# Kernel tuning notes

Measured on AMD Instinct MI355X. Metric: run time of the kernel, lower is better.

The kernel has to match this reference:

```python
import jax, jax.numpy as jnp
import numpy as np

PC = 512      # proposal_channels == conv_channels
INCH = 512    # in_channels of branch
B = 8
T = 64        # pyramid level length (feat_t) at order=0
TF = 256      # frame_level_feature length (clip_length)
KERNELS = [8, 16, 8, 4, 2, 2, 2]  # ConPoolingKernal
CLC = 498     # feature_lastclass channels (CLC + 2 == 500)
GROUPS = 32


def _gn(x, gamma, beta):
    # GroupNorm(32, C) over [B, C, L]
    Bb, C, L = x.shape
    xg = x.reshape(Bb, GROUPS, C // GROUPS, L)
    m = xg.mean(axis=(2, 3), keepdims=True)
    v = xg.var(axis=(2, 3), keepdims=True)
    xn = ((xg - m) * jax.lax.rsqrt(v + 1e-5)).reshape(Bb, C, L)
    return xn * gamma[None, :, None] + beta[None, :, None]


def _c1(x, w, b):
    # Unit1D kernel_shape=1: pointwise conv
    return jnp.einsum('bct,oc->bot', x, w) + b[None, :, None]


def _bmp(feat, segs):
    # BoundaryMaxPooling: first C/2 channels max-pooled over segs[...,0:2],
    # second C/2 over segs[...,2:4] (inclusive integer ranges, clamped).
    Bb, C, L = feat.shape
    C2 = C // 2
    pos = jnp.arange(L)
    def pool(f, s, e):
        s = jnp.clip(s, 0, L - 1)
        e = jnp.maximum(jnp.clip(e, 0, L - 1), s)
        mask = (pos[None, None, :] >= s[..., None]) & (pos[None, None, :] <= e[..., None])  # [B,T,L]
        return jnp.max(jnp.where(mask[:, None], f[:, :, None, :], -jnp.inf), axis=-1)  # [B,C2,T]
    return jnp.concatenate([pool(feat[:, :C2], segs[..., 0], segs[..., 1]),
                            pool(feat[:, C2:], segs[..., 2], segs[..., 3])], axis=1)


def _anchor_gather(feat, anc, K):
    # Vectorized per-anchor clamp/slice + nearest F.interpolate(size=K):
    # src index for output k of a slice [l, r] is l + floor(k * (r - l + 1) / K).
    Bb, C, L = feat.shape
    left = jnp.clip(anc[..., 0], 0, L)
    right = jnp.clip(anc[..., 1], 0, L)
    valid = right > left                      # empty slices -> zeros (torch branch)
    seglen = right + 1 - left
    k = jnp.arange(K)
    idx = jnp.clip(left[..., None] + (k[None, None, :] * seglen[..., None]) // K, 0, L - 1)  # [B,T,K]
    g = jax.vmap(lambda f, ix: f[:, ix])(feat, idx)   # [B,C,T,K]
    return g * valid[:, None, :, None].astype(feat.dtype)


def setup_inputs() -> dict:
    key = jax.random.key(0)
    ks = jax.random.split(key, 16)
    f32 = jnp.float32
    s = 0.02
    def w(k, shape):
        return jax.random.normal(k, shape, f32) * s
    inp = {}
    inp['feature'] = jax.random.normal(ks[0], (B, INCH, T), f32)
    inp['frame_level_feature'] = jax.random.normal(ks[1], (B, PC, TF), f32)
    inp['segments'] = jax.random.randint(ks[2], (B, T, 4), 0, T).astype(jnp.int32)
    inp['frame_segments'] = jax.random.randint(ks[3], (B, T, 4), 0, TF).astype(jnp.int32)
    inp['feature_lastclass'] = jax.random.normal(ks[4], (B, CLC, T), f32)
    inp['anchor'] = jnp.sort(jax.random.randint(ks[5], (B, T, 2), 0, T), axis=-1).astype(jnp.int32)
    inp['frame_anchor'] = jnp.sort(jax.random.randint(ks[6], (B, T, 2), 0, TF), axis=-1).astype(jnp.int32)
    inp['order'] = 0
    inp['LocResult_feature'] = jax.random.normal(ks[7], (B, 2, T), f32)
    inp['w_cur'] = w(ks[8], (PC, INCH)); inp['b_cur'] = jnp.zeros((PC,), f32)
    inp['g_cur'] = jnp.ones((PC,), f32); inp['be_cur'] = jnp.zeros((PC,), f32)
    inp['w_lr'] = w(ks[9], (2 * PC, INCH)); inp['b_lr'] = jnp.zeros((2 * PC,), f32)
    inp['g_lr'] = jnp.ones((2 * PC,), f32); inp['be_lr'] = jnp.zeros((2 * PC,), f32)
    inp['w_roi'] = w(ks[10], (PC, PC)); inp['b_roi'] = jnp.zeros((PC,), f32)
    inp['g_roi'] = jnp.ones((PC,), f32); inp['be_roi'] = jnp.zeros((PC,), f32)
    K1 = KERNELS[1]; K0 = KERNELS[0]
    inp['w_cp'] = w(ks[11], (PC, 2 * PC, K1)); inp['b_cp'] = jnp.zeros((PC,), f32)
    inp['w_cp0'] = w(ks[12], (PC, PC, K0)); inp['b_cp0'] = jnp.zeros((PC,), f32)
    CIN = 6 * PC + 500
    inp['w_prop'] = w(ks[13], (INCH, CIN)); inp['b_prop'] = jnp.zeros((INCH,), f32)
    inp['g_prop'] = jnp.ones((INCH,), f32); inp['be_prop'] = jnp.zeros((INCH,), f32)
    return inp


def reference(feature, frame_level_feature, segments, frame_segments, feature_lastclass,
              anchor, frame_anchor, order, LocResult_feature,
              w_cur, b_cur, g_cur, be_cur, w_lr, b_lr, g_lr, be_lr,
              w_roi, b_roi, g_roi, be_roi, w_cp, b_cp, w_cp0, b_cp0,
              w_prop, b_prop, g_prop, be_prop):
    relu = jax.nn.relu
    fm_short = relu(_gn(_c1(feature, w_cur, b_cur), g_cur, be_cur))           # [B,PC,T]
    feat_lr = relu(_gn(_c1(feature, w_lr, b_lr), g_lr, be_lr))                # [B,2PC,T]
    prop_feature = _bmp(feat_lr, segments)                                    # [B,2PC,T]
    prop_roi = relu(_gn(_c1(_bmp(frame_level_feature, frame_segments), w_roi, b_roi), g_roi, be_roi))
    K1 = KERNELS[order + 1]
    K0 = KERNELS[0]
    g1 = _anchor_gather(feat_lr, anchor, K1)                                  # [B,2PC,T,K1]
    con_feature = jnp.einsum('bctk,ock->bot', g1, w_cp) + b_cp[None, :, None]  # valid conv K1->1
    g0 = _anchor_gather(frame_level_feature, frame_anchor, K0)                # [B,PC,T,K0]
    frame_con = jnp.einsum('bctk,ock->bot', g0, w_cp0) + b_cp0[None, :, None]
    prop_con = relu(_gn(_c1(frame_con, w_roi, b_roi), g_roi, be_roi))
    cat = jnp.concatenate([prop_roi, prop_feature, fm_short, feature_lastclass,
                           con_feature, prop_con, LocResult_feature], axis=1)  # [B,6PC+500,T]
    out = relu(_gn(_c1(cat, w_prop, b_prop), g_prop, be_prop))                # [B,INCH,T]
    return (out, feat_lr)
```

## Files before the change

kernel.cpp:

```cpp
#include <hip/hip_runtime.h>
#include <math.h>

#define BB 8
#define CATP 3584
#define CAT_REAL 3572

typedef __attribute__((ext_vector_type(8))) short short8;
typedef __attribute__((ext_vector_type(4))) float f32x4;

__device__ inline ushort f2bf(float f) {
  union { float f; unsigned u; } x;
  x.f = f;
  return (ushort)((x.u + 0x7FFFu + ((x.u >> 16) & 1u)) >> 16);
}
__device__ inline float bf2f(unsigned us) {
  union { unsigned u; float f; } x;
  x.u = us << 16;
  return x.f;
}

template <int Cin, int Kf>
__device__ void cpT_tile(const float* __restrict__ W, ushort* __restrict__ D,
                         int nt, int cc) {
  const int tid = threadIdx.x;
  const int j = tid >> 6, l4 = (tid >> 4) & 3, l15 = tid & 15;
  const int o = nt * 64 + j * 16 + l15;
  const int cb = cc * 32 + l4 * 8;
  ushort rg[8][Kf];
#pragma unroll
  for (int q = 0; q < 8; q++) {
    const float* row = W + ((size_t)o * Cin + cb + q) * Kf;
#pragma unroll
    for (int kq = 0; kq < Kf / 4; kq++) {
      const float4 f = *(const float4*)(row + kq * 4);
      rg[q][kq * 4 + 0] = f2bf(f.x);
      rg[q][kq * 4 + 1] = f2bf(f.y);
      rg[q][kq * 4 + 2] = f2bf(f.z);
      rg[q][kq * 4 + 3] = f2bf(f.w);
    }
  }
#pragma unroll
  for (int k = 0; k < Kf; k++) {
    uint4 pk;
    pk.x = (unsigned)rg[0][k] | ((unsigned)rg[1][k] << 16);
    pk.y = (unsigned)rg[2][k] | ((unsigned)rg[3][k] << 16);
    pk.z = (unsigned)rg[4][k] | ((unsigned)rg[5][k] << 16);
    pk.w = (unsigned)rg[6][k] | ((unsigned)rg[7][k] << 16);
    *(uint4*)(D + ((size_t)(nt * Kf + k) * (Cin >> 5) + cc) * 2048 + tid * 8) = pk;
  }
}

__global__ __launch_bounds__(256) void prep_kernel(
    const float* __restrict__ w_cur, const float* __restrict__ w_lr,
    const float* __restrict__ w_roi, const float* __restrict__ w_prop,
    ushort* __restrict__ Wcomb, ushort* __restrict__ Wroi,
    ushort* __restrict__ Wprop, const float* __restrict__ w_cp,
    ushort* __restrict__ WcpT, const float* __restrict__ w_cp0,
    ushort* __restrict__ Wcp0T, const float* __restrict__ feature,
    const float* __restrict__ frame_feat, const float* __restrict__ lastcls,
    const float* __restrict__ locres, ushort* __restrict__ Ft,
    ushort* __restrict__ FfT, ushort* __restrict__ cat) {
  __shared__ float tile[64 * 65];
  const int bid = blockIdx.x;
  if (bid < 1408) {
    const int i = bid * 256 + threadIdx.x;
    const float* src;
    ushort* dst;
    int o, k8, Kc;
    bool pad = false;
    if (i < 98304) {
      o = i >> 6; k8 = i & 63; Kc = 16;
      src = (o < 512) ? (w_cur + (size_t)o * 512)
                      : (w_lr + (size_t)(o - 512) * 512);
      dst = Wcomb;
    } else if (i < 131072) {
      const int r = i - 98304;
      o = r >> 6; k8 = r & 63; Kc = 16;
      src = w_roi + (size_t)o * 512;
      dst = Wroi;
    } else {
      const int r = i - 131072;
      if (r >= 229376) return;
      o = r / 448; k8 = r % 448; Kc = 112;
      src = w_prop + (size_t)o * CAT_REAL;
      dst = Wprop;
      pad = true;
    }
    const int k = k8 * 8;
    float v[8];
    if (pad) {
#pragma unroll
      for (int q = 0; q < 8; q++) v[q] = (k + q < CAT_REAL) ? src[k + q] : 0.f;
    } else {
      const float4 f0 = *(const float4*)(src + k);
      const float4 f1 = *(const float4*)(src + k + 4);
      v[0] = f0.x; v[1] = f0.y; v[2] = f0.z; v[3] = f0.w;
      v[4] = f1.x; v[5] = f1.y; v[6] = f1.z; v[7] = f1.w;
    }
    uint4 pk;
    pk.x = (unsigned)f2bf(v[0]) | ((unsigned)f2bf(v[1]) << 16);
    pk.y = (unsigned)f2bf(v[2]) | ((unsigned)f2bf(v[3]) << 16);
    pk.z = (unsigned)f2bf(v[4]) | ((unsigned)f2bf(v[5]) << 16);
    pk.w = (unsigned)f2bf(v[6]) | ((unsigned)f2bf(v[7]) << 16);
    const int ot = o >> 6, ii = (o >> 4) & 3, l15 = o & 15;
    const int kc = k8 >> 2, l4 = k8 & 3;
    const size_t flat =
        ((((size_t)ot * Kc + kc) * 4 + ii) * 64 + l4 * 16 + l15) * 8;
    *(uint4*)(dst + flat) = pk;
    return;
  }
  if (bid < 1792) {
    const int local = bid - 1408;
    if (local < 256)
      cpT_tile<1024, 16>(w_cp, WcpT, local >> 5, local & 31);
    else {
      const int r = local - 256;
      cpT_tile<512, 8>(w_cp0, Wcp0T, r >> 4, r & 15);
    }
    return;
  }
  const int local = bid - 1792;
  const float* src;
  ushort* dst;
  int Cr, Cw, L, rs, co, cblk, lblk, b;
  if (local < 64) {
    src = feature; dst = Ft; Cr = 512; Cw = 512; L = 64; rs = 512; co = 0;
    cblk = local & 7; lblk = 0; b = local >> 3;
  } else if (local < 320) {
    const int r = local - 64;
    src = frame_feat; dst = FfT; Cr = 512; Cw = 512; L = 256; rs = 512; co = 0;
    cblk = r & 7; lblk = (r >> 3) & 3; b = r >> 5;
  } else if (local < 384) {
    const int r = local - 320;
    src = lastcls; dst = cat; Cr = 498; Cw = 498; L = 64; rs = CATP; co = 2048;
    cblk = r & 7; lblk = 0; b = r >> 3;
  } else {
    const int r = local - 384;
    src = locres; dst = cat; Cr = 2; Cw = 14; L = 64; rs = CATP; co = 3570;
    cblk = 0; lblk = 0; b = r;
  }
  const int c0 = cblk * 64, l0 = lblk * 64;
  for (int e = threadIdx.x; e < 4096; e += 256) {
    const int cc = e >> 6, ll = e & 63;
    const int c = c0 + cc;
    tile[cc * 65 + ll] = (c < Cr) ? src[((size_t)b * Cr + c) * L + l0 + ll] : 0.f;
  }
  __syncthreads();
  for (int e = threadIdx.x; e < 4096; e += 256) {
    const int ll = e >> 6, cc = e & 63;
    const int c = c0 + cc;
    if (c < Cw)
      dst[((size_t)b * L + l0 + ll) * rs + co + c] = f2bf(tile[cc * 65 + ll]);
  }
}

__global__ __launch_bounds__(256) void gemm_gn_seg_kernel(
    int nblk0,
    const ushort* __restrict__ X0, const ushort* __restrict__ W0,
    const float* __restrict__ b0, const float* __restrict__ g0,
    const float* __restrict__ e0, int Kp0, int cs0, float* of0, int om0,
    ushort* co0, int cst0, int coff0,
    const ushort* __restrict__ X1, const ushort* __restrict__ W1,
    const float* __restrict__ b1, const float* __restrict__ g1,
    const float* __restrict__ e1, int Kp1, int cs1, float* of1, int om1,
    ushort* co1, int cst1, int coff1) {
  const int bx = blockIdx.x;
  const bool s1 = bx >= nblk0;
  const ushort* Xt = s1 ? X1 : X0;
  const ushort* Wb = s1 ? W1 : W0;
  const float* bias = s1 ? b1 : b0;
  const float* gamma = s1 ? g1 : g0;
  const float* beta = s1 ? e1 : e0;
  const int Kp = s1 ? Kp1 : Kp0;
  const int cpgShift = s1 ? cs1 : cs0;
  float* outF = s1 ? of1 : of0;
  const int outFM = s1 ? om1 : om0;
  ushort* catOut = s1 ? co1 : co0;
  const int catStride = s1 ? cst1 : cst0;
  const int chOff = s1 ? coff1 : coff0;
  const int o0 = (s1 ? bx - nblk0 : bx) * 64;

  const int b = blockIdx.y;
  const int w = threadIdx.x >> 6;
  const int lane = threadIdx.x & 63;
  const int l15 = lane & 15, l4 = lane >> 4;
  const int wk = Kp >> 2;
  const int kbeg = w * wk, kend = kbeg + wk;

  f32x4 acc[4][4] = {};
  const ushort* wbase = Wb + (size_t)(o0 >> 6) * (Kp >> 5) * 2048 + lane * 8;
  const ushort* bp[4];
#pragma unroll
  for (int j = 0; j < 4; j++)
    bp[j] = Xt + (size_t)(b * 64 + j * 16 + l15) * Kp + l4 * 8;

  for (int k = kbeg; k < kend; k += 32) {
    const int kc = k >> 5;
    short8 a[4], x[4];
#pragma unroll
    for (int i = 0; i < 4; i++)
      a[i] = *(const short8*)(wbase + ((size_t)kc * 4 + i) * 512);
#pragma unroll
    for (int j = 0; j < 4; j++) x[j] = *(const short8*)(bp[j] + k);
#pragma unroll
    for (int i = 0; i < 4; i++)
#pragma unroll
      for (int j = 0; j < 4; j++)
        acc[i][j] = __builtin_amdgcn_mfma_f32_16x16x32_bf16(a[i], x[j],
                                                            acc[i][j], 0, 0, 0);
  }

  __shared__ float red[64 * 65];
  for (int ww = 0; ww < 4; ww++) {
    __syncthreads();
    if (w == ww) {
#pragma unroll
      for (int i = 0; i < 4; i++)
#pragma unroll
        for (int j = 0; j < 4; j++)
#pragma unroll
          for (int r = 0; r < 4; r++) {
            const int m = i * 16 + l4 * 4 + r;
            const int n = j * 16 + l15;
            if (ww == 0)
              red[m * 65 + n] = acc[i][j][r] + bias[o0 + m];
            else
              red[m * 65 + n] += acc[i][j][r];
          }
    }
  }
  __syncthreads();

  const int cpg = 1 << cpgShift;
  const int ngroups = 64 >> cpgShift;
  __shared__ float rs[4], rss[4], gmean[4], grstd[4];
  for (int gi = 0; gi < ngroups; gi++) {
    float s = 0.f, ss = 0.f;
    const int nel = cpg << 6;
    for (int e = threadIdx.x; e < nel; e += 256) {
      const float v = red[((gi << cpgShift) + (e >> 6)) * 65 + (e & 63)];
      s += v;
      ss += v * v;
    }
#pragma unroll
    for (int off = 32; off > 0; off >>= 1) {
      s += __shfl_down(s, off);
      ss += __shfl_down(ss, off);
    }
    if (lane == 0) { rs[w] = s; rss[w] = ss; }
    __syncthreads();
    if (threadIdx.x == 0) {
      const float ts = rs[0] + rs[1] + rs[2] + rs[3];
      const float tss = rss[0] + rss[1] + rss[2] + rss[3];
      const float mean = ts / (float)nel;
      const float var = tss / (float)nel - mean * mean;
      gmean[gi] = mean;
      grstd[gi] = rsqrtf(var + 1e-5f);
    }
    __syncthreads();
  }

  if (outF) {
    for (int e = threadIdx.x; e < 4096; e += 256) {
      const int m = e >> 6, n = e & 63;
      const int gi = m >> cpgShift;
      const int c = o0 + m;
      float v = (red[m * 65 + n] - gmean[gi]) * grstd[gi] * gamma[c] + beta[c];
      v = fmaxf(v, 0.f);
      outF[((size_t)b * outFM + c) * 64 + n] = v;
    }
  }
  if (catOut) {
    for (int e = threadIdx.x; e < 4096; e += 256) {
      const int n = e >> 6, m = e & 63;
      const int gi = m >> cpgShift;
      const int c = o0 + m;
      float v = (red[m * 65 + n] - gmean[gi]) * grstd[gi] * gamma[c] + beta[c];
      v = fmaxf(v, 0.f);
      catOut[((size_t)(b * 64) + n) * catStride + chOff + c] = f2bf(v);
    }
  }
}

__global__ __launch_bounds__(256) void gemm_part_kernel(
    const ushort* __restrict__ Xt, const ushort* __restrict__ Wb,
    float* __restrict__ P) {
  const int ot = blockIdx.x;
  const int b = blockIdx.y;
  const int kz = blockIdx.z;
  const int w = threadIdx.x >> 6;
  const int lane = threadIdx.x & 63;
  const int l15 = lane & 15, l4 = lane >> 4;
  const int kbeg = kz * 896 + w * 224;
  const int kend = kbeg + 224;

  f32x4 acc[4][4] = {};
  const ushort* wbase = Wb + (size_t)ot * (CATP >> 5) * 2048 + lane * 8;
  const ushort* bp[4];
#pragma unroll
  for (int j = 0; j < 4; j++)
    bp[j] = Xt + (size_t)(b * 64 + j * 16 + l15) * CATP + l4 * 8;

  for (int k = kbeg; k < kend; k += 32) {
    const int kc = k >> 5;
    short8 a[4], x[4];
#pragma unroll
    for (int i = 0; i < 4; i++)
      a[i] = *(const short8*)(wbase + ((size_t)kc * 4 + i) * 512);
#pragma unroll
    for (int j = 0; j < 4; j++) x[j] = *(const short8*)(bp[j] + k);
#pragma unroll
    for (int i = 0; i < 4; i++)
#pragma unroll
      for (int j = 0; j < 4; j++)
        acc[i][j] = __builtin_amdgcn_mfma_f32_16x16x32_bf16(a[i], x[j],
                                                            acc[i][j], 0, 0, 0);
  }

  __shared__ float red[64 * 65];
  for (int ww = 0; ww < 4; ww++) {
    __syncthreads();
    if (w == ww) {
#pragma unroll
      for (int i = 0; i < 4; i++)
#pragma unroll
        for (int j = 0; j < 4; j++)
#pragma unroll
          for (int r = 0; r < 4; r++) {
            const int m = i * 16 + l4 * 4 + r;
            const int n = j * 16 + l15;
            if (ww == 0)
              red[m * 65 + n] = acc[i][j][r];
            else
              red[m * 65 + n] += acc[i][j][r];
          }
    }
  }
  __syncthreads();
  float* Pp = P + (((size_t)kz * BB + b) * 512 + ot * 64) * 64;
  for (int e = threadIdx.x; e < 4096; e += 256) Pp[e] = red[(e >> 6) * 65 + (e & 63)];
}

__global__ __launch_bounds__(256) void reduce_gn_kernel(
    const float* __restrict__ P, const float* __restrict__ bias,
    const float* __restrict__ gamma, const float* __restrict__ beta,
    float* __restrict__ outF) {
  const int ot = blockIdx.x;
  const int b = blockIdx.y;
  const int o0 = ot * 64;
  const int w = threadIdx.x >> 6;
  const int lane = threadIdx.x & 63;
  __shared__ float red[64 * 65];
  for (int e = threadIdx.x; e < 4096; e += 256) {
    const int m = e >> 6, n = e & 63;
    float s = bias[o0 + m];
#pragma unroll
    for (int z = 0; z < 4; z++)
      s += P[(((size_t)z * BB + b) * 512 + o0 + m) * 64 + n];
    red[m * 65 + n] = s;
  }
  __syncthreads();
  __shared__ float rs[4], rss[4], gmean[4], grstd[4];
  for (int gi = 0; gi < 4; gi++) {
    float s = 0.f, ss = 0.f;
    for (int e = threadIdx.x; e < 1024; e += 256) {
      const float v = red[((gi << 4) + (e >> 6)) * 65 + (e & 63)];
      s += v;
      ss += v * v;
    }
#pragma unroll
    for (int off = 32; off > 0; off >>= 1) {
      s += __shfl_down(s, off);
      ss += __shfl_down(ss, off);
    }
    if (lane == 0) { rs[w] = s; rss[w] = ss; }
    __syncthreads();
    if (threadIdx.x == 0) {
      const float ts = rs[0] + rs[1] + rs[2] + rs[3];
      const float tss = rss[0] + rss[1] + rss[2] + rss[3];
      const float mean = ts / 1024.f;
      const float var = tss / 1024.f - mean * mean;
      gmean[gi] = mean;
      grstd[gi] = rsqrtf(var + 1e-5f);
    }
    __syncthreads();
  }
  for (int e = threadIdx.x; e < 4096; e += 256) {
    const int m = e >> 6, n = e & 63;
    const int gi = m >> 4;
    const int c = o0 + m;
    float v = (red[m * 65 + n] - gmean[gi]) * grstd[gi] * gamma[c] + beta[c];
    outF[((size_t)b * 512 + c) * 64 + n] = fmaxf(v, 0.f);
  }
}

template <int C, int L>
__device__ void bmp_body(const ushort* __restrict__ Xt,
                         const int* __restrict__ segs, ushort* __restrict__ Y,
                         int rowStride, int chOff, float2 (*pmax)[512]) {
  constexpr int C2 = C / 2;
  constexpr int P2 = C2 / 2;
  constexpr int CH = P2 / 64;
  const int t = blockIdx.x;
  const int b = blockIdx.y;
  const int w = threadIdx.x >> 6;
  const int lane = threadIdx.x & 63;
  const int* sg = segs + ((size_t)b * 64 + t) * 4;
  const ushort* Xb = Xt + (size_t)b * L * C;
#pragma unroll
  for (int h = 0; h < 2; h++) {
    const int s = min(max(sg[2 * h], 0), L - 1);
    const int e = max(min(max(sg[2 * h + 1], 0), L - 1), s);
#pragma unroll
    for (int q = 0; q < CH; q++) {
      const int p = q * 64 + lane;
      const ushort* base = Xb + h * C2 + 2 * p;
      float a0 = -INFINITY, a1 = -INFINITY;
      float c0 = -INFINITY, c1 = -INFINITY;
      int l = s + w;
      for (; l + 4 <= e; l += 8) {
        const unsigned u0 = *(const unsigned*)(base + (size_t)l * C);
        const unsigned u1 = *(const unsigned*)(base + (size_t)(l + 4) * C);
        a0 = fmaxf(a0, bf2f(u0 & 0xffffu));
        a1 = fmaxf(a1, bf2f(u0 >> 16));
        c0 = fmaxf(c0, bf2f(u1 & 0xffffu));
        c1 = fmaxf(c1, bf2f(u1 >> 16));
      }
      if (l <= e) {
        const unsigned u0 = *(const unsigned*)(base + (size_t)l * C);
        a0 = fmaxf(a0, bf2f(u0 & 0xffffu));
        a1 = fmaxf(a1, bf2f(u0 >> 16));
      }
      pmax[w][h * P2 + p] = make_float2(fmaxf(a0, c0), fmaxf(a1, c1));
    }
  }
  __syncthreads();
  for (int idx = threadIdx.x; idx < 2 * P2; idx += 256) {
    float2 m = pmax[0][idx];
#pragma unroll
    for (int ww = 1; ww < 4; ww++) {
      const float2 v = pmax[ww][idx];
      m.x = fmaxf(m.x, v.x);
      m.y = fmaxf(m.y, v.y);
    }
    const unsigned o = (unsigned)f2bf(m.x) | ((unsigned)f2bf(m.y) << 16);
    *(unsigned*)(Y + ((size_t)(b * 64) + t) * rowStride + chOff + 2 * idx) = o;
  }
}

__global__ __launch_bounds__(256) void bmp_dual_kernel(
    const ushort* __restrict__ FlrT, const int* __restrict__ segments,
    ushort* __restrict__ cat, const ushort* __restrict__ FfT,
    const int* __restrict__ frame_segs, ushort* __restrict__ XbmpT) {
  __shared__ float2 pm[4][512];
  if (blockIdx.z == 0)
    bmp_body<1024, 64>(FlrT, segments, cat, CATP, 512, pm);
  else
    bmp_body<512, 256>(FfT, frame_segs, XbmpT, 512, 0, pm);
}

template <int Kf, int L, int Cin>
__device__ void anchor_mfma_body(const ushort* __restrict__ src,
                                 const int* __restrict__ anc,
                                 const ushort* __restrict__ Wt,
                                 float* __restrict__ P, int slice, float* red) {
  const int nt = blockIdx.x;
  const int b = blockIdx.y;
  const int w = threadIdx.x >> 6;
  const int lane = threadIdx.x & 63;
  const int l15 = lane & 15, l4 = lane >> 4;
  const int kz = slice >> 1, chalf = slice & 1;
  const int k = kz * 4 + w;
  const int cbase = chalf * (Cin / 2);

  const ushort* rp[4];
#pragma unroll
  for (int i = 0; i < 4; i++) {
    const int t = i * 16 + l15;
    const int a0 = anc[((size_t)b * 64 + t) * 2 + 0];
    const int a1 = anc[((size_t)b * 64 + t) * 2 + 1];
    const int left = min(max(a0, 0), L);
    const int right = min(max(a1, 0), L);
    const int seglen = right + 1 - left;
    const int ix = min(max(left + (k * seglen) / Kf, 0), L - 1);
    rp[i] = src + ((size_t)b * L + ix) * Cin + cbase + l4 * 8;
  }
  const ushort* wb = Wt + (size_t)(nt * Kf + k) * (Cin >> 5) * 2048 + lane * 8;

  f32x4 acc[4][4] = {};
  for (int c0 = 0; c0 < Cin / 2; c0 += 32) {
    const int cc = (cbase + c0) >> 5;
    short8 a[4], bb[4];
#pragma unroll
    for (int i = 0; i < 4; i++) a[i] = *(const short8*)(rp[i] + c0);
#pragma unroll
    for (int j = 0; j < 4; j++)
      bb[j] = *(const short8*)(wb + ((size_t)cc * 4 + j) * 512);
#pragma unroll
    for (int i = 0; i < 4; i++)
#pragma unroll
      for (int j = 0; j < 4; j++)
        acc[i][j] = __builtin_amdgcn_mfma_f32_16x16x32_bf16(a[i], bb[j],
                                                            acc[i][j], 0, 0, 0);
  }

  for (int ww = 0; ww < 4; ww++) {
    __syncthreads();
    if (w == ww) {
#pragma unroll
      for (int i = 0; i < 4; i++)
#pragma unroll
        for (int j = 0; j < 4; j++)
#pragma unroll
          for (int r = 0; r < 4; r++) {
            const int m = i * 16 + l4 * 4 + r;
            const int n = j * 16 + l15;
            if (ww == 0)
              red[m * 65 + n] = acc[i][j][r];
            else
              red[m * 65 + n] += acc[i][j][r];
          }
    }
  }
  __syncthreads();
  float* Pp = P + (((size_t)slice * BB + b) * 512 + nt * 64) * 64;
  for (int e = threadIdx.x; e < 4096; e += 256) {
    const int n = e >> 6, m = e & 63;
    Pp[e] = red[m * 65 + n];
  }
}

__global__ __launch_bounds__(256) void anchor_mfma_dual_kernel(
    const ushort* __restrict__ FlrT, const int* __restrict__ anchor,
    const ushort* __restrict__ WcpT, float* __restrict__ P1,
    const ushort* __restrict__ FfT, const int* __restrict__ frame_anchor,
    const ushort* __restrict__ Wcp0T, float* __restrict__ P0) {
  __shared__ float red[64 * 65];
  const int z = blockIdx.z;
  if (z < 8)
    anchor_mfma_body<16, 64, 1024>(FlrT, anchor, WcpT, P1, z, red);
  else
    anchor_mfma_body<8, 256, 512>(FfT, frame_anchor, Wcp0T, P0, z - 8, red);
}

__device__ void anchor_reduce_body(const float* __restrict__ P, int ks,
                                   const float* __restrict__ bias,
                                   const int* __restrict__ anc, int L,
                                   ushort* __restrict__ Y, int rowStride,
                                   int chOff, float* tile, float* sval) {
  const int o0 = blockIdx.x * 64;
  const int b = blockIdx.y;
  if (threadIdx.x < 64) {
    const int t = threadIdx.x;
    const int a0 = anc[((size_t)b * 64 + t) * 2 + 0];
    const int a1 = anc[((size_t)b * 64 + t) * 2 + 1];
    const int left = min(max(a0, 0), L);
    const int right = min(max(a1, 0), L);
    sval[t] = (right > left) ? 1.f : 0.f;
  }
  __syncthreads();
  for (int e = threadIdx.x; e < 4096; e += 256) {
    const int nl = e >> 6, m = e & 63;
    const int n = o0 + nl;
    float s = 0.f;
    for (int z = 0; z < ks; z++)
      s += P[(((size_t)z * BB + b) * 512 + n) * 64 + m];
    tile[nl * 65 + m] = s * sval[m] + bias[n];
  }
  __syncthreads();
  for (int e = threadIdx.x; e < 4096; e += 256) {
    const int m = e >> 6, nl = e & 63;
    Y[((size_t)(b * 64) + m) * rowStride + chOff + o0 + nl] =
        f2bf(tile[nl * 65 + m]);
  }
}

__global__ __launch_bounds__(256) void anchor_reduce_dual_kernel(
    const float* __restrict__ P1, const float* __restrict__ b_cp,
    const int* __restrict__ anchor, ushort* __restrict__ cat,
    const float* __restrict__ P0, const float* __restrict__ b_cp0,
    const int* __restrict__ frame_anchor, ushort* __restrict__ FconT) {
  __shared__ float tile[64 * 65];
  __shared__ float sval[64];
  if (blockIdx.z == 0)
    anchor_reduce_body(P1, 8, b_cp, anchor, 64, cat, CATP, 2546, tile, sval);
  else
    anchor_reduce_body(P0, 4, b_cp0, frame_anchor, 256, FconT, 512, 0, tile, sval);
}

extern "C" void kernel_launch(void* const* d_in, const int* in_sizes, int n_in,
                              void* d_out, int out_size, void* d_ws,
                              size_t ws_size, hipStream_t stream) {
  const float* feature      = (const float*)d_in[0];
  const float* frame_feat   = (const float*)d_in[1];
  const int*   segments     = (const int*)d_in[2];
  const int*   frame_segs   = (const int*)d_in[3];
  const float* feat_lastcls = (const float*)d_in[4];
  const int*   anchor       = (const int*)d_in[5];
  const int*   frame_anchor = (const int*)d_in[6];
  const float* locres       = (const float*)d_in[8];
  const float* w_cur  = (const float*)d_in[9];
  const float* b_cur  = (const float*)d_in[10];
  const float* g_cur  = (const float*)d_in[11];
  const float* be_cur = (const float*)d_in[12];
  const float* w_lr   = (const float*)d_in[13];
  const float* b_lr   = (const float*)d_in[14];
  const float* g_lr   = (const float*)d_in[15];
  const float* be_lr  = (const float*)d_in[16];
  const float* w_roi  = (const float*)d_in[17];
  const float* b_roi  = (const float*)d_in[18];
  const float* g_roi  = (const float*)d_in[19];
  const float* be_roi = (const float*)d_in[20];
  const float* w_cp   = (const float*)d_in[21];
  const float* b_cp   = (const float*)d_in[22];
  const float* w_cp0  = (const float*)d_in[23];
  const float* b_cp0  = (const float*)d_in[24];
  const float* w_prop = (const float*)d_in[25];
  const float* b_prop = (const float*)d_in[26];
  const float* g_prop = (const float*)d_in[27];
  const float* be_prop= (const float*)d_in[28];

  float* out_main = (float*)d_out;
  float* feat_lr  = (float*)d_out + BB * 512 * 64;

  ushort* cat_t  = (ushort*)d_ws;
  ushort* Ft     = cat_t + 1835008;
  ushort* XbmpT  = Ft + 262144;
  ushort* FconT  = XbmpT + 262144;
  ushort* Wcomb  = FconT + 262144;
  ushort* Wroi   = Wcomb + 786432;
  ushort* Wprop  = Wroi + 262144;
  ushort* WcpT   = Wprop + 1835008;
  ushort* Wcp0T  = WcpT + 8388608;
  ushort* FlrT   = Wcp0T + 2097152;
  ushort* FfT    = FlrT + 524288;
  float*  P1     = (float*)(FfT + 1048576);
  float*  P0     = P1 + 2097152;
  float*  P9     = P0 + 1048576;

  prep_kernel<<<2184, 256, 0, stream>>>(
      w_cur, w_lr, w_roi, w_prop, Wcomb, Wroi, Wprop, w_cp, WcpT, w_cp0,
      Wcp0T, feature, frame_feat, feat_lastcls, locres, Ft, FfT, cat_t);

  gemm_gn_seg_kernel<<<dim3(24, BB), 256, 0, stream>>>(
      8,
      Ft, Wcomb, b_cur, g_cur, be_cur, 512, 4, nullptr, 0, cat_t, CATP, 1536,
      Ft, Wcomb + 512 * 512, b_lr, g_lr, be_lr, 512, 5, feat_lr, 1024, FlrT,
      1024, 0);

  bmp_dual_kernel<<<dim3(64, BB, 2), 256, 0, stream>>>(
      FlrT, segments, cat_t, FfT, frame_segs, XbmpT);

  anchor_mfma_dual_kernel<<<dim3(8, BB, 12), 256, 0, stream>>>(
      FlrT, anchor, WcpT, P1, FfT, frame_anchor, Wcp0T, P0);

  anchor_reduce_dual_kernel<<<dim3(8, BB, 2), 256, 0, stream>>>(
      P1, b_cp, anchor, cat_t, P0, b_cp0, frame_anchor, FconT);

  gemm_gn_seg_kernel<<<dim3(16, BB), 256, 0, stream>>>(
      8,
      XbmpT, Wroi, b_roi, g_roi, be_roi, 512, 4, nullptr, 0, cat_t, CATP, 0,
      FconT, Wroi, b_roi, g_roi, be_roi, 512, 4, nullptr, 0, cat_t, CATP, 3058);

  gemm_part_kernel<<<dim3(8, BB, 4), 256, 0, stream>>>(cat_t, Wprop, P9);

  reduce_gn_kernel<<<dim3(8, BB), 256, 0, stream>>>(
      P9, b_prop, g_prop, be_prop, out_main);
}
```

Before: 266.7 us.

## Regroup pipeline stages into dependency-level fused kernels to cut launches

Replaces the separate gemm_gn, bmp, anchor_mfma, anchor_reduce and second gemm_gn launches with three level kernels. Each level kernel dispatches independent stages by blockIdx.z. Stages now run together as soon as their inputs exist: the frame-anchor MFMA runs beside the first pointwise GEMM, and the frame-anchor reduce runs beside the BMP and feature-anchor MFMA. This removes two kernel launches and their serialization gaps and lets small stages fill idle CUs. In exchange, shared memory becomes one union sized for the largest stage, and some grid blocks exit immediately without doing work.

```diff
diff --git a/kernel.cpp b/kernel.cpp
--- a/kernel.cpp
+++ b/kernel.cpp
@@ -4,6 +4,7 @@
 #define BB 8
 #define CATP 3584
 #define CAT_REAL 3572
+#define SH_FLOATS 4240
 
 typedef __attribute__((ext_vector_type(8))) short short8;
 typedef __attribute__((ext_vector_type(4))) float f32x4;
@@ -154,33 +155,17 @@
   }
 }
 
-__global__ __launch_bounds__(256) void gemm_gn_seg_kernel(
-    int nblk0,
-    const ushort* __restrict__ X0, const ushort* __restrict__ W0,
-    const float* __restrict__ b0, const float* __restrict__ g0,
-    const float* __restrict__ e0, int Kp0, int cs0, float* of0, int om0,
-    ushort* co0, int cst0, int coff0,
-    const ushort* __restrict__ X1, const ushort* __restrict__ W1,
-    const float* __restrict__ b1, const float* __restrict__ g1,
-    const float* __restrict__ e1, int Kp1, int cs1, float* of1, int om1,
-    ushort* co1, int cst1, int coff1) {
-  const int bx = blockIdx.x;
-  const bool s1 = bx >= nblk0;
-  const ushort* Xt = s1 ? X1 : X0;
-  const ushort* Wb = s1 ? W1 : W0;
-  const float* bias = s1 ? b1 : b0;
-  const float* gamma = s1 ? g1 : g0;
-  const float* beta = s1 ? e1 : e0;
-  const int Kp = s1 ? Kp1 : Kp0;
-  const int cpgShift = s1 ? cs1 : cs0;
-  float* outF = s1 ? of1 : of0;
-  const int outFM = s1 ? om1 : om0;
-  ushort* catOut = s1 ? co1 : co0;
-  const int catStride = s1 ? cst1 : cst0;
-  const int chOff = s1 ? coff1 : coff0;
-  const int o0 = (s1 ? bx - nblk0 : bx) * 64;
-
-  const int b = blockIdx.y;
+__device__ void gemm_gn_body(
+    const ushort* __restrict__ Xt, const ushort* __restrict__ Wb,
+    const float* __restrict__ bias, const float* __restrict__ gamma,
+    const float* __restrict__ beta, int Kp, int cpgShift, float* outF,
+    int outFM, ushort* catOut, int catStride, int chOff, int o0, int b,
+    float* sh) {
+  float* red = sh;
+  float* rs = sh + 4160;
+  float* rss = sh + 4164;
+  float* gmean = sh + 4168;
+  float* grstd = sh + 4172;
   const int w = threadIdx.x >> 6;
   const int lane = threadIdx.x & 63;
   const int l15 = lane & 15, l4 = lane >> 4;
@@ -210,7 +195,6 @@
                                                             acc[i][j], 0, 0, 0);
   }
 
-  __shared__ float red[64 * 65];
   for (int ww = 0; ww < 4; ww++) {
     __syncthreads();
     if (w == ww) {
@@ -233,7 +217,6 @@
 
   const int cpg = 1 << cpgShift;
   const int ngroups = 64 >> cpgShift;
-  __shared__ float rs[4], rss[4], gmean[4], grstd[4];
   for (int gi = 0; gi < ngroups; gi++) {
     float s = 0.f, ss = 0.f;
     const int nel = cpg << 6;
@@ -282,122 +265,10 @@
   }
 }
 
-__global__ __launch_bounds__(256) void gemm_part_kernel(
-    const ushort* __restrict__ Xt, const ushort* __restrict__ Wb,
-    float* __restrict__ P) {
-  const int ot = blockIdx.x;
-  const int b = blockIdx.y;
-  const int kz = blockIdx.z;
-  const int w = threadIdx.x >> 6;
-  const int lane = threadIdx.x & 63;
-  const int l15 = lane & 15, l4 = lane >> 4;
-  const int kbeg = kz * 896 + w * 224;
-  const int kend = kbeg + 224;
-
-  f32x4 acc[4][4] = {};
-  const ushort* wbase = Wb + (size_t)ot * (CATP >> 5) * 2048 + lane * 8;
-  const ushort* bp[4];
-#pragma unroll
-  for (int j = 0; j < 4; j++)
-    bp[j] = Xt + (size_t)(b * 64 + j * 16 + l15) * CATP + l4 * 8;
-
-  for (int k = kbeg; k < kend; k += 32) {
-    const int kc = k >> 5;
-    short8 a[4], x[4];
-#pragma unroll
-    for (int i = 0; i < 4; i++)
-      a[i] = *(const short8*)(wbase + ((size_t)kc * 4 + i) * 512);
-#pragma unroll
-    for (int j = 0; j < 4; j++) x[j] = *(const short8*)(bp[j] + k);
-#pragma unroll
-    for (int i = 0; i < 4; i++)
-#pragma unroll
-      for (int j = 0; j < 4; j++)
-        acc[i][j] = __builtin_amdgcn_mfma_f32_16x16x32_bf16(a[i], x[j],
-                                                            acc[i][j], 0, 0, 0);
-  }
-
-  __shared__ float red[64 * 65];
-  for (int ww = 0; ww < 4; ww++) {
-    __syncthreads();
-    if (w == ww) {
-#pragma unroll
-      for (int i = 0; i < 4; i++)
-#pragma unroll
-        for (int j = 0; j < 4; j++)
-#pragma unroll
-          for (int r = 0; r < 4; r++) {
-            const int m = i * 16 + l4 * 4 + r;
-            const int n = j * 16 + l15;
-            if (ww == 0)
-              red[m * 65 + n] = acc[i][j][r];
-            else
-              red[m * 65 + n] += acc[i][j][r];
-          }
-    }
-  }
-  __syncthreads();
-  float* Pp = P + (((size_t)kz * BB + b) * 512 + ot * 64) * 64;
-  for (int e = threadIdx.x; e < 4096; e += 256) Pp[e] = red[(e >> 6) * 65 + (e & 63)];
-}
-
-__global__ __launch_bounds__(256) void reduce_gn_kernel(
-    const float* __restrict__ P, const float* __restrict__ bias,
-    const float* __restrict__ gamma, const float* __restrict__ beta,
-    float* __restrict__ outF) {
-  const int ot = blockIdx.x;
-  const int b = blockIdx.y;
-  const int o0 = ot * 64;
-  const int w = threadIdx.x >> 6;
-  const int lane = threadIdx.x & 63;
-  __shared__ float red[64 * 65];
-  for (int e = threadIdx.x; e < 4096; e += 256) {
-    const int m = e >> 6, n = e & 63;
-    float s = bias[o0 + m];
-#pragma unroll
-    for (int z = 0; z < 4; z++)
-      s += P[(((size_t)z * BB + b) * 512 + o0 + m) * 64 + n];
-    red[m * 65 + n] = s;
-  }
-  __syncthreads();
-  __shared__ float rs[4], rss[4], gmean[4], grstd[4];
-  for (int gi = 0; gi < 4; gi++) {
-    float s = 0.f, ss = 0.f;
-    for (int e = threadIdx.x; e < 1024; e += 256) {
-      const float v = red[((gi << 4) + (e >> 6)) * 65 + (e & 63)];
-      s += v;
-      ss += v * v;
-    }
-#pragma unroll
-    for (int off = 32; off > 0; off >>= 1) {
-      s += __shfl_down(s, off);
-      ss += __shfl_down(ss, off);
-    }
-    if (lane == 0) { rs[w] = s; rss[w] = ss; }
-    __syncthreads();
-    if (threadIdx.x == 0) {
-      const float ts = rs[0] + rs[1] + rs[2] + rs[3];
-      const float tss = rss[0] + rss[1] + rss[2] + rss[3];
-      const float mean = ts / 1024.f;
-      const float var = tss / 1024.f - mean * mean;
-      gmean[gi] = mean;
-      grstd[gi] = rsqrtf(var + 1e-5f);
-    }
-    __syncthreads();
-  }
-  for (int e = threadIdx.x; e < 4096; e += 256) {
-    const int m = e >> 6, n = e & 63;
-    const int gi = m >> 4;
-    const int c = o0 + m;
-    float v = (red[m * 65 + n] - gmean[gi]) * grstd[gi] * gamma[c] + beta[c];
-    outF[((size_t)b * 512 + c) * 64 + n] = fmaxf(v, 0.f);
-  }
-}
-
 template <int C, int L>
 __device__ void bmp_body(const ushort* __restrict__ Xt,
                          const int* __restrict__ segs, ushort* __restrict__ Y,
-                         int rowStride, int chOff, float2 (*pmax)[512]) {
+                         int rowStride, int chOff, float2* pmax ) {
   constexpr int C2 = C / 2;
   constexpr int P2 = C2 / 2;
   constexpr int CH = P2 / 64;
@@ -431,40 +302,29 @@
         a0 = fmaxf(a0, bf2f(u0 & 0xffffu));
         a1 = fmaxf(a1, bf2f(u0 >> 16));
       }
-      pmax[w][h * P2 + p] = make_float2(fmaxf(a0, c0), fmaxf(a1, c1));
+      pmax[w * 512 + h * P2 + p] = make_float2(fmaxf(a0, c0), fmaxf(a1, c1));
     }
   }
   __syncthreads();
   for (int idx = threadIdx.x; idx < 2 * P2; idx += 256) {
-    float2 m = pmax[0][idx];
+    float2 m = pmax[idx];
 #pragma unroll
     for (int ww = 1; ww < 4; ww++) {
-      const float2 v = pmax[ww][idx];
+      const float2 v = pmax[ww * 512 + idx];
       m.x = fmaxf(m.x, v.x);
       m.y = fmaxf(m.y, v.y);
     }
     const unsigned o = (unsigned)f2bf(m.x) | ((unsigned)f2bf(m.y) << 16);
     *(unsigned*)(Y + ((size_t)(b * 64) + t) * rowStride + chOff + 2 * idx) = o;
   }
-}
-
-__global__ __launch_bounds__(256) void bmp_dual_kernel(
-    const ushort* __restrict__ FlrT, const int* __restrict__ segments,
-    ushort* __restrict__ cat, const ushort* __restrict__ FfT,
-    const int* __restrict__ frame_segs, ushort* __restrict__ XbmpT) {
-  __shared__ float2 pm[4][512];
-  if (blockIdx.z == 0)
-    bmp_body<1024, 64>(FlrT, segments, cat, CATP, 512, pm);
-  else
-    bmp_body<512, 256>(FfT, frame_segs, XbmpT, 512, 0, pm);
 }
 
 template <int Kf, int L, int Cin>
 __device__ void anchor_mfma_body(const ushort* __restrict__ src,
                                  const int* __restrict__ anc,
                                  const ushort* __restrict__ Wt,
-                                 float* __restrict__ P, int slice, float* red) {
-  const int nt = blockIdx.x;
+                                 float* __restrict__ P, int nt, int slice,
+                                 float* red) {
   const int b = blockIdx.y;
   const int w = threadIdx.x >> 6;
   const int lane = threadIdx.x & 63;
@@ -530,25 +390,13 @@
   }
 }
 
-__global__ __launch_bounds__(256) void anchor_mfma_dual_kernel(
-    const ushort* __restrict__ FlrT, const int* __restrict__ anchor,
-    const ushort* __restrict__ WcpT, float* __restrict__ P1,
-    const ushort* __restrict__ FfT, const int* __restrict__ frame_anchor,
-    const ushort* __restrict__ Wcp0T, float* __restrict__ P0) {
-  __shared__ float red[64 * 65];
-  const int z = blockIdx.z;
-  if (z < 8)
-    anchor_mfma_body<16, 64, 1024>(FlrT, anchor, WcpT, P1, z, red);
-  else
-    anchor_mfma_body<8, 256, 512>(FfT, frame_anchor, Wcp0T, P0, z - 8, red);
-}
-
 __device__ void anchor_reduce_body(const float* __restrict__ P, int ks,
                                    const float* __restrict__ bias,
                                    const int* __restrict__ anc, int L,
                                    ushort* __restrict__ Y, int rowStride,
-                                   int chOff, float* tile, float* sval) {
-  const int o0 = blockIdx.x * 64;
+                                   int chOff, int ot, float* tile,
+                                   float* sval) {
+  const int o0 = ot * 64;
   const int b = blockIdx.y;
   if (threadIdx.x < 64) {
     const int t = threadIdx.x;
@@ -575,17 +423,187 @@
   }
 }
 
-__global__ __launch_bounds__(256) void anchor_reduce_dual_kernel(
+__global__ __launch_bounds__(256) void level2_kernel(
+    const ushort* __restrict__ Ft, const ushort* __restrict__ Wcomb,
+    const float* __restrict__ b_cur, const float* __restrict__ g_cur,
+    const float* __restrict__ be_cur, const float* __restrict__ b_lr,
+    const float* __restrict__ g_lr, const float* __restrict__ be_lr,
+    float* __restrict__ feat_lr, ushort* __restrict__ FlrT,
+    ushort* __restrict__ cat, const ushort* __restrict__ FfT,
+    const int* __restrict__ frame_anchor, const ushort* __restrict__ Wcp0T,
+    float* __restrict__ P0) {
+  __shared__ float sh[SH_FLOATS];
+  const int x = blockIdx.x;
+  if (blockIdx.z == 0) {
+    if (x >= 24) return;
+    if (x < 8)
+      gemm_gn_body(Ft, Wcomb, b_cur, g_cur, be_cur, 512, 4, nullptr, 0, cat,
+                   CATP, 1536, x * 64, blockIdx.y, sh);
+    else
+      gemm_gn_body(Ft, Wcomb + 512 * 512, b_lr, g_lr, be_lr, 512, 5, feat_lr,
+                   1024, FlrT, 1024, 0, (x - 8) * 64, blockIdx.y, sh);
+  } else {
+    anchor_mfma_body<8, 256, 512>(FfT, frame_anchor, Wcp0T, P0, x & 7, x >> 3,
+                                  sh);
+  }
+}
+
+__global__ __launch_bounds__(256) void level3_kernel(
+    const ushort* __restrict__ FlrT, const int* __restrict__ segments,
+    ushort* __restrict__ cat, const ushort* __restrict__ FfT,
+    const int* __restrict__ frame_segs, ushort* __restrict__ XbmpT,
+    const int* __restrict__ anchor, const ushort* __restrict__ WcpT,
+    float* __restrict__ P1, const float* __restrict__ P0,
+    const float* __restrict__ b_cp0, const int* __restrict__ frame_anchor,
+    ushort* __restrict__ FconT) {
+  __shared__ float sh[SH_FLOATS];
+  const int x = blockIdx.x;
+  const int z = blockIdx.z;
+  if (z == 0) {
+    bmp_body<1024, 64>(FlrT, segments, cat, CATP, 512, (float2*)sh);
+  } else if (z == 1) {
+    bmp_body<512, 256>(FfT, frame_segs, XbmpT, 512, 0, (float2*)sh);
+  } else if (z == 2) {
+    anchor_mfma_body<16, 64, 1024>(FlrT, anchor, WcpT, P1, x & 7, x >> 3, sh);
+  } else {
+    if (x >= 8) return;
+    anchor_reduce_body(P0, 4, b_cp0, frame_anchor, 256, FconT, 512, 0, x, sh,
+                       sh + 4160);
+  }
+}
+
+__global__ __launch_bounds__(256) void level4_kernel(
     const float* __restrict__ P1, const float* __restrict__ b_cp,
     const int* __restrict__ anchor, ushort* __restrict__ cat,
-    const float* __restrict__ P0, const float* __restrict__ b_cp0,
-    const int* __restrict__ frame_anchor, ushort* __restrict__ FconT) {
-  __shared__ float tile[64 * 65];
-  __shared__ float sval[64];
-  if (blockIdx.z == 0)
-    anchor_reduce_body(P1, 8, b_cp, anchor, 64, cat, CATP, 2546, tile, sval);
-  else
-    anchor_reduce_body(P0, 4, b_cp0, frame_anchor, 256, FconT, 512, 0, tile, sval);
+    const ushort* __restrict__ XbmpT, const ushort* __restrict__ FconT,
+    const ushort* __restrict__ Wroi, const float* __restrict__ b_roi,
+    const float* __restrict__ g_roi, const float* __restrict__ be_roi) {
+  __shared__ float sh[SH_FLOATS];
+  const int x = blockIdx.x;
+  const int z = blockIdx.z;
+  if (z == 0) {
+    anchor_reduce_body(P1, 8, b_cp, anchor, 64, cat, CATP, 2546, x, sh,
+                       sh + 4160);
+  } else if (z == 1) {
+    gemm_gn_body(XbmpT, Wroi, b_roi, g_roi, be_roi, 512, 4, nullptr, 0, cat,
+                 CATP, 0, x * 64, blockIdx.y, sh);
+  } else {
+    gemm_gn_body(FconT, Wroi, b_roi, g_roi, be_roi, 512, 4, nullptr, 0, cat,
+                 CATP, 3058, x * 64, blockIdx.y, sh);
+  }
+}
+
+__global__ __launch_bounds__(256) void gemm_part_kernel(
+    const ushort* __restrict__ Xt, const ushort* __restrict__ Wb,
+    float* __restrict__ P) {
+  const int ot = blockIdx.x;
+  const int b = blockIdx.y;
+  const int kz = blockIdx.z;
+  const int w = threadIdx.x >> 6;
+  const int lane = threadIdx.x & 63;
+  const int l15 = lane & 15, l4 = lane >> 4;
+  const int kbeg = kz * 896 + w * 224;
+  const int kend = kbeg + 224;
+
+  f32x4 acc[4][4] = {};
+  const ushort* wbase = Wb + (size_t)ot * (CATP >> 5) * 2048 + lane * 8;
+  const ushort* bp[4];
+#pragma unroll
+  for (int j = 0; j < 4; j++)
+    bp[j] = Xt + (size_t)(b * 64 + j * 16 + l15) * CATP + l4 * 8;
+
+  for (int k = kbeg; k < kend; k += 32) {
+    const int kc = k >> 5;
+    short8 a[4], x[4];
+#pragma unroll
+    for (int i = 0; i < 4; i++)
+      a[i] = *(const short8*)(wbase + ((size_t)kc * 4 + i) * 512);
+#pragma unroll
+    for (int j = 0; j < 4; j++) x[j] = *(const short8*)(bp[j] + k);
+#pragma unroll
+    for (int i = 0; i < 4; i++)
+#pragma unroll
+      for (int j = 0; j < 4; j++)
+        acc[i][j] = __builtin_amdgcn_mfma_f32_16x16x32_bf16(a[i], x[j],
+                                                            acc[i][j], 0, 0, 0);
+  }
+
+  __shared__ float red[64 * 65];
+  for (int ww = 0; ww < 4; ww++) {
+    __syncthreads();
+    if (w == ww) {
+#pragma unroll
+      for (int i = 0; i < 4; i++)
+#pragma unroll
+        for (int j = 0; j < 4; j++)
+#pragma unroll
+          for (int r = 0; r < 4; r++) {
+            const int m = i * 16 + l4 * 4 + r;
+            const int n = j * 16 + l15;
+            if (ww == 0)
+              red[m * 65 + n] = acc[i][j][r];
+            else
+              red[m * 65 + n] += acc[i][j][r];
+          }
+    }
+  }
+  __syncthreads();
+  float* Pp = P + (((size_t)kz * BB + b) * 512 + ot * 64) * 64;
+  for (int e = threadIdx.x; e < 4096; e += 256)
+    Pp[e] = red[(e >> 6) * 65 + (e & 63)];
+}
+
+__global__ __launch_bounds__(256) void reduce_gn_kernel(
+    const float* __restrict__ P, const float* __restrict__ bias,
+    const float* __restrict__ gamma, const float* __restrict__ beta,
+    float* __restrict__ outF) {
+  const int ot = blockIdx.x;
+  const int b = blockIdx.y;
+  const int o0 = ot * 64;
+  const int w = threadIdx.x >> 6;
+  const int lane = threadIdx.x & 63;
+  __shared__ float red[64 * 65];
+  for (int e = threadIdx.x; e < 4096; e += 256) {
+    const int m = e >> 6, n = e & 63;
+    float s = bias[o0 + m];
+#pragma unroll
+    for (int z = 0; z < 4; z++)
+      s += P[(((size_t)z * BB + b) * 512 + o0 + m) * 64 + n];
+    red[m * 65 + n] = s;
+  }
+  __syncthreads();
+  __shared__ float rs[4], rss[4], gmean[4], grstd[4];
+  for (int gi = 0; gi < 4; gi++) {
+    float s = 0.f, ss = 0.f;
+    for (int e = threadIdx.x; e < 1024; e += 256) {
+      const float v = red[((gi << 4) + (e >> 6)) * 65 + (e & 63)];
+      s += v;
+      ss += v * v;
+    }
+#pragma unroll
+    for (int off = 32; off > 0; off >>= 1) {
+      s += __shfl_down(s, off);
+      ss += __shfl_down(ss, off);
+    }
+    if (lane == 0) { rs[w] = s; rss[w] = ss; }
+    __syncthreads();
+    if (threadIdx.x == 0) {
+      const float ts = rs[0] + rs[1] + rs[2] + rs[3];
+      const float tss = rss[0] + rss[1] + rss[2] + rss[3];
+      const float mean = ts / 1024.f;
+      const float var = tss / 1024.f - mean * mean;
+      gmean[gi] = mean;
+      grstd[gi] = rsqrtf(var + 1e-5f);
+    }
+    __syncthreads();
+  }
+  for (int e = threadIdx.x; e < 4096; e += 256) {
+    const int m = e >> 6, n = e & 63;
+    const int gi = m >> 4;
+    const int c = o0 + m;
+    float v = (red[m * 65 + n] - gmean[gi]) * grstd[gi] * gamma[c] + beta[c];
+    outF[((size_t)b * 512 + c) * 64 + n] = fmaxf(v, 0.f);
+  }
 }
 
 extern "C" void kernel_launch(void* const* d_in, const int* in_sizes, int n_in,
@@ -642,25 +660,16 @@
       w_cur, w_lr, w_roi, w_prop, Wcomb, Wroi, Wprop, w_cp, WcpT, w_cp0,
       Wcp0T, feature, frame_feat, feat_lastcls, locres, Ft, FfT, cat_t);
 
-  gemm_gn_seg_kernel<<<dim3(24, BB), 256, 0, stream>>>(
-      8,
-      Ft, Wcomb, b_cur, g_cur, be_cur, 512, 4, nullptr, 0, cat_t, CATP, 1536,
-      Ft, Wcomb + 512 * 512, b_lr, g_lr, be_lr, 512, 5, feat_lr, 1024, FlrT,
-      1024, 0);
-
-  bmp_dual_kernel<<<dim3(64, BB, 2), 256, 0, stream>>>(
-      FlrT, segments, cat_t, FfT, frame_segs, XbmpT);
-
-  anchor_mfma_dual_kernel<<<dim3(8, BB, 12), 256, 0, stream>>>(
-      FlrT, anchor, WcpT, P1, FfT, frame_anchor, Wcp0T, P0);
-
-  anchor_reduce_dual_kernel<<<dim3(8, BB, 2), 256, 0, stream>>>(
-      P1, b_cp, anchor, cat_t, P0, b_cp0, frame_anchor, FconT);
-
-  gemm_gn_seg_kernel<<<dim3(16, BB), 256, 0, stream>>>(
-      8,
-      XbmpT, Wroi, b_roi, g_roi, be_roi, 512, 4, nullptr, 0, cat_t, CATP, 0,
-      FconT, Wroi, b_roi, g_roi, be_roi, 512, 4, nullptr, 0, cat_t, CATP, 3058);
+  level2_kernel<<<dim3(32, BB, 2), 256, 0, stream>>>(
+      Ft, Wcomb, b_cur, g_cur, be_cur, b_lr, g_lr, be_lr, feat_lr, FlrT,
+      cat_t, FfT, frame_anchor, Wcp0T, P0);
+
+  level3_kernel<<<dim3(64, BB, 4), 256, 0, stream>>>(
+      FlrT, segments, cat_t, FfT, frame_segs, XbmpT, anchor, WcpT, P1, P0,
+      b_cp0, frame_anchor, FconT);
+
+  level4_kernel<<<dim3(8, BB, 3), 256, 0, stream>>>(
+      P1, b_cp, anchor, cat_t, XbmpT, FconT, Wroi, b_roi, g_roi, be_roi);
 
   gemm_part_kernel<<<dim3(8, BB, 4), 256, 0, stream>>>(cat_t, Wprop, P9);
 
```

Measured after the change: 274.3 us. 2.9% more time.

## Process two batches per anchor MFMA block and split channels into quarters

Applied to the files above, without the earlier changes.

Each block of the anchor-gather MFMA kernel now computes two batch elements, so every weight fragment it loads feeds twice as many MFMAs. The channel dimension is split into four slices instead of two, which keeps the block count up; the kernel loop is fully unrolled. In exchange there are twice as many partial buffers for the reduce kernel to sum, a larger workspace, and higher register pressure from the doubled accumulators.

```diff
diff --git a/kernel.cpp b/kernel.cpp
--- a/kernel.cpp
+++ b/kernel.cpp
@@ -338,7 +338,8 @@
   }
   __syncthreads();
   float* Pp = P + (((size_t)kz * BB + b) * 512 + ot * 64) * 64;
-  for (int e = threadIdx.x; e < 4096; e += 256) Pp[e] = red[(e >> 6) * 65 + (e & 63)];
+  for (int e = threadIdx.x; e < 4096; e += 256)
+    Pp[e] = red[(e >> 6) * 65 + (e & 63)];
 }
 
 __global__ __launch_bounds__(256) void reduce_gn_kernel(
@@ -465,68 +466,85 @@
                                  const ushort* __restrict__ Wt,
                                  float* __restrict__ P, int slice, float* red) {
   const int nt = blockIdx.x;
-  const int b = blockIdx.y;
+  const int b0 = blockIdx.y * 2;
   const int w = threadIdx.x >> 6;
   const int lane = threadIdx.x & 63;
   const int l15 = lane & 15, l4 = lane >> 4;
-  const int kz = slice >> 1, chalf = slice & 1;
+  const int kz = slice >> 2, cq = slice & 3;
   const int k = kz * 4 + w;
-  const int cbase = chalf * (Cin / 2);
-
-  const ushort* rp[4];
-#pragma unroll
-  for (int i = 0; i < 4; i++) {
-    const int t = i * 16 + l15;
-    const int a0 = anc[((size_t)b * 64 + t) * 2 + 0];
-    const int a1 = anc[((size_t)b * 64 + t) * 2 + 1];
-    const int left = min(max(a0, 0), L);
-    const int right = min(max(a1, 0), L);
-    const int seglen = right + 1 - left;
-    const int ix = min(max(left + (k * seglen) / Kf, 0), L - 1);
-    rp[i] = src + ((size_t)b * L + ix) * Cin + cbase + l4 * 8;
+  const int cbase = cq * (Cin / 4);
+  constexpr int NC = (Cin / 4) / 32;
+
+  const ushort* rp[2][4];
+#pragma unroll
+  for (int bsel = 0; bsel < 2; bsel++) {
+    const int b = b0 + bsel;
+#pragma unroll
+    for (int i = 0; i < 4; i++) {
+      const int t = i * 16 + l15;
+      const int a0 = anc[((size_t)b * 64 + t) * 2 + 0];
+      const int a1 = anc[((size_t)b * 64 + t) * 2 + 1];
+      const int left = min(max(a0, 0), L);
+      const int right = min(max(a1, 0), L);
+      const int seglen = right + 1 - left;
+      const int ix = min(max(left + (k * seglen) / Kf, 0), L - 1);
+      rp[bsel][i] = src + ((size_t)b * L + ix) * Cin + cbase + l4 * 8;
+    }
   }
   const ushort* wb = Wt + (size_t)(nt * Kf + k) * (Cin >> 5) * 2048 + lane * 8;
 
-  f32x4 acc[4][4] = {};
-  for (int c0 = 0; c0 < Cin / 2; c0 += 32) {
+  f32x4 acc[2][4][4] = {};
+#pragma unroll
+  for (int it = 0; it < NC; it++) {
+    const int c0 = it * 32;
     const int cc = (cbase + c0) >> 5;
-    short8 a[4], bb[4];
-#pragma unroll
-    for (int i = 0; i < 4; i++) a[i] = *(const short8*)(rp[i] + c0);
+    short8 bb[4];
 #pragma unroll
     for (int j = 0; j < 4; j++)
       bb[j] = *(const short8*)(wb + ((size_t)cc * 4 + j) * 512);
-#pragma unroll
-    for (int i = 0; i < 4; i++)
-#pragma unroll
-      for (int j = 0; j < 4; j++)
-        acc[i][j] = __builtin_amdgcn_mfma_f32_16x16x32_bf16(a[i], bb[j],
-                                                            acc[i][j], 0, 0, 0);
-  }
-
-  for (int ww = 0; ww < 4; ww++) {
+    short8 aa[2][4];
+#pragma unroll
+    for (int bsel = 0; bsel < 2; bsel++)
+#pragma unroll
+      for (int i = 0; i < 4; i++)
+        aa[bsel][i] = *(const short8*)(rp[bsel][i] + c0);
+#pragma unroll
+    for (int bsel = 0; bsel < 2; bsel++)
+#pragma unroll
+      for (int i = 0; i < 4; i++)
+#pragma unroll
+        for (int j = 0; j < 4; j++)
+          acc[bsel][i][j] = __builtin_amdgcn_mfma_f32_16x16x32_bf16(
+              aa[bsel][i], bb[j], acc[bsel][i][j], 0, 0, 0);
+  }
+
+#pragma unroll
+  for (int bsel = 0; bsel < 2; bsel++) {
+    for (int ww = 0; ww < 4; ww++) {
+      __syncthreads();
+      if (w == ww) {
+#pragma unroll
+        for (int i = 0; i < 4; i++)
+#pragma unroll
+          for (int j = 0; j < 4; j++)
+#pragma unroll
+            for (int r = 0; r < 4; r++) {
+              const int m = i * 16 + l4 * 4 + r;
+              const int n = j * 16 + l15;
+              if (ww == 0)
+                red[m * 65 + n] = acc[bsel][i][j][r];
+              else
+                red[m * 65 + n] += acc[bsel][i][j][r];
+            }
+      }
+    }
     __syncthreads();
-    if (w == ww) {
-#pragma unroll
-      for (int i = 0; i < 4; i++)
-#pragma unroll
-        for (int j = 0; j < 4; j++)
-#pragma unroll
-          for (int r = 0; r < 4; r++) {
-            const int m = i * 16 + l4 * 4 + r;
-            const int n = j * 16 + l15;
-            if (ww == 0)
-              red[m * 65 + n] = acc[i][j][r];
-            else
-              red[m * 65 + n] += acc[i][j][r];
-          }
-    }
-  }
-  __syncthreads();
-  float* Pp = P + (((size_t)slice * BB + b) * 512 + nt * 64) * 64;
-  for (int e = threadIdx.x; e < 4096; e += 256) {
-    const int n = e >> 6, m = e & 63;
-    Pp[e] = red[m * 65 + n];
+    const int b = b0 + bsel;
+    float* Pp = P + (((size_t)slice * BB + b) * 512 + nt * 64) * 64;
+    for (int e = threadIdx.x; e < 4096; e += 256) {
+      const int n = e >> 6, m = e & 63;
+      Pp[e] = red[m * 65 + n];
+    }
   }
 }
 
@@ -537,10 +555,10 @@
     const ushort* __restrict__ Wcp0T, float* __restrict__ P0) {
   __shared__ float red[64 * 65];
   const int z = blockIdx.z;
-  if (z < 8)
+  if (z < 16)
     anchor_mfma_body<16, 64, 1024>(FlrT, anchor, WcpT, P1, z, red);
   else
-    anchor_mfma_body<8, 256, 512>(FfT, frame_anchor, Wcp0T, P0, z - 8, red);
+    anchor_mfma_body<8, 256, 512>(FfT, frame_anchor, Wcp0T, P0, z - 16, red);
 }
 
 __device__ void anchor_reduce_body(const float* __restrict__ P, int ks,
@@ -583,9 +601,9 @@
   __shared__ float tile[64 * 65];
   __shared__ float sval[64];
   if (blockIdx.z == 0)
-    anchor_reduce_body(P1, 8, b_cp, anchor, 64, cat, CATP, 2546, tile, sval);
+    anchor_reduce_body(P1, 16, b_cp, anchor, 64, cat, CATP, 2546, tile, sval);
   else
-    anchor_reduce_body(P0, 4, b_cp0, frame_anchor, 256, FconT, 512, 0, tile, sval);
+    anchor_reduce_body(P0, 8, b_cp0, frame_anchor, 256, FconT, 512, 0, tile, sval);
 }
 
 extern "C" void kernel_launch(void* const* d_in, const int* in_sizes, int n_in,
@@ -635,8 +653,8 @@
   ushort* FlrT   = Wcp0T + 2097152;
   ushort* FfT    = FlrT + 524288;
   float*  P1     = (float*)(FfT + 1048576);
-  float*  P0     = P1 + 2097152;
-  float*  P9     = P0 + 1048576;
+  float*  P0     = P1 + 4194304;
+  float*  P9     = P0 + 2097152;
 
   prep_kernel<<<2184, 256, 0, stream>>>(
       w_cur, w_lr, w_roi, w_prop, Wcomb, Wroi, Wprop, w_cp, WcpT, w_cp0,
@@ -651,7 +669,7 @@
   bmp_dual_kernel<<<dim3(64, BB, 2), 256, 0, stream>>>(
       FlrT, segments, cat_t, FfT, frame_segs, XbmpT);
 
-  anchor_mfma_dual_kernel<<<dim3(8, BB, 12), 256, 0, stream>>>(
+  anchor_mfma_dual_kernel<<<dim3(8, 4, 24), 256, 0, stream>>>(
       FlrT, anchor, WcpT, P1, FfT, frame_anchor, Wcp0T, P0);
 
   anchor_reduce_dual_kernel<<<dim3(8, BB, 2), 256, 0, stream>>>(
```

Measured after the change: 288.7 us. 1.08x slower.
